# Kernel optimization log

Measured on AMD Instinct MI355X. Metric: run time of the kernel, lower is better.

## Reference

```python
import jax, jax.numpy as jnp
import numpy as np

N = 100000   # num nodes
E = 1200000  # num edges
D = 64       # hidden_channel == middle_channel
ALPHA = 0.5
LN_EPS = 1e-5


def setup_inputs() -> dict:
    key = jax.random.key(0)
    ks = jax.random.split(key, 8)
    z = jax.random.normal(ks[0], (N, D), jnp.float32)
    x = jax.random.normal(ks[1], (N, D), jnp.float32)
    edge_index = jax.random.randint(ks[2], (2, E), 0, N)
    norm_factor = jax.random.uniform(ks[3], (N, 1), jnp.float32)  # >0 a.s.
    s = 0.1
    W = jax.random.normal(ks[4], (D, D), jnp.float32) * s    # nn.Linear(hidden, hidden, bias=False).weight
    U_w = jax.random.normal(ks[5], (D, D), jnp.float32) * s  # nn.Linear(hidden, middle).weight
    U_b = jax.random.normal(ks[6], (D,), jnp.float32) * s    # nn.Linear(hidden, middle).bias
    ln_gamma = jnp.ones((D,), jnp.float32)
    ln_beta = jnp.zeros((D,), jnp.float32)
    return dict(z=z, x=x, edge_index=edge_index, norm_factor=norm_factor,
                W=W, U_w=U_w, U_b=U_b, ln_gamma=ln_gamma, ln_beta=ln_beta)


def reference(z, x, edge_index, norm_factor, W, U_w, U_b, ln_gamma, ln_beta):
    row, col = edge_index[0], edge_index[1]
    # rescale=True: degree = 1/norm_factor with inf -> 0 (safe division)
    safe_nf = jnp.where(norm_factor > 0, norm_factor, 1.0)
    degree = jnp.where(norm_factor > 0, 1.0 / safe_nf, 0.0)  # [N,1]
    # double_linear=True: W(z) + degree * U(x), then graph-norm scale
    WzUx = z @ W.T + degree * (x @ U_w.T + U_b)  # [N,D]
    WzUx = norm_factor * WzUx
    # edge diff (gather), act + LayerNorm (batch=None path)
    e = WzUx[row] - WzUx[col]                    # [E,D]
    e = jax.nn.relu(e)
    mu = jnp.mean(e, axis=-1, keepdims=True)
    var = jnp.var(e, axis=-1, keepdims=True)
    e = (e - mu) * jax.lax.rsqrt(var + LN_EPS) * ln_gamma + ln_beta
    # double scatter_add aggregation
    new_z = jax.ops.segment_sum(e * norm_factor[row], row, num_segments=N)
    new_z = new_z - jax.ops.segment_sum(e * norm_factor[col], col, num_segments=N)
    # -F.linear(new_z, W.t()) == -(new_z @ W)
    new_z = -(new_z @ W)
    # dropout p=0.0 -> identity
    return ALPHA * new_z + (1.0 - ALPHA) * z
```

## Files before the change

kernel.cpp:

```cpp
#include <hip/hip_runtime.h>

#define D 64
#define LN_EPS 1e-5f
#define ALPHA 0.5f

#define GSH 8
#define GBN 256
#define NSUB 8
#define TILE 2048
#define CAPS 1280
#define CAPQ 1792
#define OVF_CAP 131072
#define MAXBUCK 400
#define WZB 2048

__device__ __forceinline__ unsigned xcc_id() {
    unsigned v;
    asm volatile("s_getreg_b32 %0, hwreg(HW_REG_XCC_ID)" : "=s"(v));
    return v & (NSUB - 1);
}

__device__ __forceinline__ unsigned short f2bf(float f) {
    unsigned u = __float_as_uint(f);
    u += 0x7FFF + ((u >> 16) & 1);
    return (unsigned short)(u >> 16);
}
__device__ __forceinline__ float bf2f(unsigned short h) {
    return __uint_as_float(((unsigned)h) << 16);
}

template <int CTRL>
__device__ __forceinline__ float dpp_rotadd(float v) {
    int p = __builtin_amdgcn_update_dpp(0, __float_as_int(v), CTRL, 0xF, 0xF, true);
    return v + __int_as_float(p);
}

__global__ __launch_bounds__(256) void front_kernel(
    const int* __restrict__ row, const int* __restrict__ col,
    int* __restrict__ gcur, int* __restrict__ data,
    int* __restrict__ ovf_cnt, int2* __restrict__ ovf,
    int E, int nbuck, int sb,
    const float* __restrict__ z, const float* __restrict__ x,
    const float* __restrict__ nf, const float* __restrict__ W,
    const float* __restrict__ Uw, const float* __restrict__ Ub,
    unsigned short* __restrict__ wzux, int N)
{
    __shared__ int cnt[MAXBUCK];
    __shared__ int gbase[MAXBUCK];
    const int t = threadIdx.x;

    if ((int)blockIdx.x < sb) {
        const int e0 = blockIdx.x * TILE;
        const int e1 = min(e0 + TILE, E);
        const unsigned sub = xcc_id();

        for (int i = t; i < nbuck; i += 256) cnt[i] = 0;
        __syncthreads();

        for (int e = e0 + t; e < e1; e += 256) {
            atomicAdd(&cnt[row[e] >> GSH], 1);
            atomicAdd(&cnt[col[e] >> GSH], 1);
        }
        __syncthreads();

        for (int b = t; b < nbuck; b += 256) {
            int c = cnt[b];
            gbase[b] = (c > 0) ? atomicAdd(&gcur[b * NSUB + sub], c) : 0;
        }
        __syncthreads();

        for (int e = e0 + t; e < e1; e += 256) {
            int r = row[e], c = col[e];
            {
                int b = r >> GSH;
                int s = atomicSub(&cnt[b], 1) - 1;
                int pos = gbase[b] + s;
                int rec = (c << 9) | ((r & (GBN - 1)) << 1);
                if (pos < CAPS) data[(b * NSUB + (int)sub) * CAPS + pos] = rec;
                else { int o = atomicAdd(ovf_cnt, 1);
                       if (o < OVF_CAP) ovf[o] = make_int2(b, rec); }
            }
            {
                int b = c >> GSH;
                int s = atomicSub(&cnt[b], 1) - 1;
                int pos = gbase[b] + s;
                int rec = (r << 9) | ((c & (GBN - 1)) << 1) | 1;
                if (pos < CAPS) data[(b * NSUB + (int)sub) * CAPS + pos] = rec;
                else { int o = atomicAdd(ovf_cnt, 1);
                       if (o < OVF_CAP) ovf[o] = make_int2(b, rec); }
            }
        }
    } else {
        const int wb   = blockIdx.x - sb;
        const int lane = t & 63;
        const int wid  = t >> 6;
        const int par   = (wb >> 3) & 1;
        const int chunk = (wb & 7) | ((wb >> 4) << 3);
        const int half = lane >> 5;
        const int d    = par * 32 + (lane & 31);

        const float* M = half ? Uw : W;
        float4 wreg[16];
        {
            const float4* wr = (const float4*)(M + (size_t)d * D);
#pragma unroll
            for (int i = 0; i < 16; ++i) wreg[i] = wr[i];
        }
        const float ub = Ub[d];
        const float* base_src = half ? x : z;

        const int start = chunk * 4 + wid;
        const int step  = (WZB >> 1) * 4;

        for (int n = start; n < N; n += step) {
            const int un = __builtin_amdgcn_readfirstlane(n);
            const float4* src = (const float4*)(base_src + (size_t)un * D);
            float a0 = 0.f, a1 = 0.f, a2 = 0.f, a3 = 0.f;
#pragma unroll
            for (int c = 0; c < 16; ++c) {
                float4 v = src[c];
                a0 = fmaf(v.x, wreg[c].x, a0);
                a1 = fmaf(v.y, wreg[c].y, a1);
                a2 = fmaf(v.z, wreg[c].z, a2);
                a3 = fmaf(v.w, wreg[c].w, a3);
            }
            float acc = (a0 + a1) + (a2 + a3);
            float other = __shfl_xor(acc, 32);
            if (half == 0) {
                float nfv = nf[un];
                float deg = (nfv > 0.f) ? (1.f / nfv) : 0.f;
                wzux[(size_t)un * D + d] = f2bf(nfv * (acc + deg * (other + ub)));
            }
        }
    }
}

__global__ __launch_bounds__(256) void bucket_sort_agg_kernel(
    const unsigned short* __restrict__ wzux,
    const int* __restrict__ gcur, const int* __restrict__ data,
    const int* __restrict__ ovf_cnt, const int2* __restrict__ ovf,
    const float* __restrict__ nf,
    const float4* __restrict__ gamma4, const float4* __restrict__ beta4,
    float4* __restrict__ out4, int N)
{
    __shared__ int sorted[CAPQ];
    __shared__ int offs[65];
    __shared__ int curs[64];

    const int blk    = blockIdx.x;
    const int base   = blk << 6;
    const int cntN   = min(64, N - base);
    const int bucket = blk >> 2;
    const int q      = blk & 3;
    const int t      = threadIdx.x;

    if (t < 65) offs[t] = 0;
    __syncthreads();

    const int ocnt = min(*ovf_cnt, OVF_CAP);

    for (int sub = 0; sub < NSUB; ++sub) {
        const int cs = min(gcur[bucket * NSUB + sub], CAPS);
        const int* p = &data[(bucket * NSUB + sub) * CAPS];
        for (int i = t; i < cs; i += 256) {
            int l8 = (p[i] >> 1) & (GBN - 1);
            if ((l8 >> 6) == q) atomicAdd(&offs[(l8 & 63) + 1], 1);
        }
    }
    for (int i = t; i < ocnt; i += 256) {
        int2 v = ovf[i];
        int l8 = (v.y >> 1) & (GBN - 1);
        if (v.x == bucket && (l8 >> 6) == q) atomicAdd(&offs[(l8 & 63) + 1], 1);
    }
    __syncthreads();

    if (t < 64) {
        int v = offs[t + 1];
#pragma unroll
        for (int off = 1; off < 64; off <<= 1) {
            int u = __shfl_up(v, off);
            if (t >= off) v += u;
        }
        offs[t + 1] = v;
    }
    __syncthreads();
    if (t < 64) curs[t] = offs[t];
    __syncthreads();

    for (int sub = 0; sub < NSUB; ++sub) {
        const int cs = min(gcur[bucket * NSUB + sub], CAPS);
        const int* p = &data[(bucket * NSUB + sub) * CAPS];
        for (int i = t; i < cs; i += 256) {
            int rec = p[i];
            int l8 = (rec >> 1) & (GBN - 1);
            if ((l8 >> 6) == q) {
                int pos = atomicAdd(&curs[l8 & 63], 1);
                if (pos < CAPQ) sorted[pos] = rec;
            }
        }
    }
    for (int i = t; i < ocnt; i += 256) {
        int2 v = ovf[i];
        int l8 = (v.y >> 1) & (GBN - 1);
        if (v.x == bucket && (l8 >> 6) == q) {
            int pos = atomicAdd(&curs[l8 & 63], 1);
            if (pos < CAPQ) sorted[pos] = v.y;
        }
    }
    __syncthreads();

    const int lane = t & 63;
    const int wid  = t >> 6;
    const int g = lane >> 4;
    const int l = lane & 15;
    const float4 gm = gamma4[l];
    const float4 bt = beta4[l];
    const ushort4* wz4 = (const ushort4*)wzux;

    for (int local = wid; local < cntN; local += 4) {
        const int s = min(offs[local], CAPQ);
        const int e = min(offs[local + 1], CAPQ);
        const int n = base + local;
        ushort4 sh = wz4[n * 16 + l];
        const float4 self = make_float4(bf2f(sh.x), bf2f(sh.y),
                                        bf2f(sh.z), bf2f(sh.w));
        float4 acc = make_float4(0.f, 0.f, 0.f, 0.f);

#define PROC2(ENT, H)                                                        \
        {                                                                    \
            int ent = (ENT);                                                 \
            float sgn = (ent & 1) ? -1.f : 1.f;                              \
            float4 o = make_float4(bf2f((H).x), bf2f((H).y),                 \
                                   bf2f((H).z), bf2f((H).w));                \
            float r0 = fmaxf(sgn * (self.x - o.x), 0.f);                     \
            float r1 = fmaxf(sgn * (self.y - o.y), 0.f);                     \
            float r2 = fmaxf(sgn * (self.z - o.z), 0.f);                     \
            float r3 = fmaxf(sgn * (self.w - o.w), 0.f);                     \
            float ss = r0 + r1 + r2 + r3;                                    \
            float sq = r0 * r0 + r1 * r1 + r2 * r2 + r3 * r3;                \
            ss = dpp_rotadd<0x128>(ss);  sq = dpp_rotadd<0x128>(sq);         \
            ss = dpp_rotadd<0x124>(ss);  sq = dpp_rotadd<0x124>(sq);         \
            ss = dpp_rotadd<0x122>(ss);  sq = dpp_rotadd<0x122>(sq);         \
            ss = dpp_rotadd<0x121>(ss);  sq = dpp_rotadd<0x121>(sq);         \
            float mu   = ss * (1.f / 64.f);                                  \
            float var  = sq * (1.f / 64.f) - mu * mu;                        \
            float rstd = rsqrtf(var + LN_EPS);                               \
            acc.x += sgn * ((r0 - mu) * rstd * gm.x + bt.x);                 \
            acc.y += sgn * ((r1 - mu) * rstd * gm.y + bt.y);                 \
            acc.z += sgn * ((r2 - mu) * rstd * gm.z + bt.z);                 \
            acc.w += sgn * ((r3 - mu) * rstd * gm.w + bt.w);                 \
        }

        int i = s + g;
        for (; i + 12 < e; i += 16) {
            int e0 = sorted[i];
            int e1 = sorted[i + 4];
            int e2 = sorted[i + 8];
            int e3 = sorted[i + 12];
            ushort4 h0 = wz4[(e0 >> 9) * 16 + l];
            ushort4 h1 = wz4[(e1 >> 9) * 16 + l];
            ushort4 h2 = wz4[(e2 >> 9) * 16 + l];
            ushort4 h3 = wz4[(e3 >> 9) * 16 + l];
            PROC2(e0, h0);
            PROC2(e1, h1);
            PROC2(e2, h2);
            PROC2(e3, h3);
        }
        for (; i < e; i += 4) {
            int e0 = sorted[i];
            ushort4 h0 = wz4[(e0 >> 9) * 16 + l];
            PROC2(e0, h0);
        }
#undef PROC2

#pragma unroll
        for (int m = 16; m < 64; m <<= 1) {
            acc.x += __shfl_xor(acc.x, m);
            acc.y += __shfl_xor(acc.y, m);
            acc.z += __shfl_xor(acc.z, m);
            acc.w += __shfl_xor(acc.w, m);
        }

        if (g == 0) {
            float nfv = nf[n];
            out4[n * 16 + l] = make_float4(acc.x * nfv, acc.y * nfv,
                                           acc.z * nfv, acc.w * nfv);
        }
    }
}

__global__ __launch_bounds__(256) void out_kernel(
    const float* accv, const float* __restrict__ z,
    const float* __restrict__ W, float* out, int N)
{
    const int lane = threadIdx.x & 63;
    const int wid  = threadIdx.x >> 6;

    float wcol[D];
#pragma unroll
    for (int k = 0; k < D; ++k) wcol[k] = W[k * D + lane];

    for (int n = blockIdx.x * 4 + wid; n < N; n += gridDim.x * 4) {
        const int un = __builtin_amdgcn_readfirstlane(n);
        const float4* ar = (const float4*)(accv + (size_t)un * D);
        float a0 = 0.f, a1 = 0.f, a2 = 0.f, a3 = 0.f;
#pragma unroll
        for (int c = 0; c < 16; ++c) {
            float4 a = ar[c];
            a0 = fmaf(a.x, wcol[c * 4 + 0], a0);
            a1 = fmaf(a.y, wcol[c * 4 + 1], a1);
            a2 = fmaf(a.z, wcol[c * 4 + 2], a2);
            a3 = fmaf(a.w, wcol[c * 4 + 3], a3);
        }
        float acc = (a0 + a1) + (a2 + a3);
        out[(size_t)un * D + lane] =
            (1.0f - ALPHA) * z[(size_t)un * D + lane] - ALPHA * acc;
    }
}

extern "C" void kernel_launch(void* const* d_in, const int* in_sizes, int n_in,
                              void* d_out, int out_size, void* d_ws, size_t ws_size,
                              hipStream_t stream) {
    const float* z     = (const float*)d_in[0];
    const float* x     = (const float*)d_in[1];
    const int*   ei    = (const int*)d_in[2];
    const float* nf    = (const float*)d_in[3];
    const float* W     = (const float*)d_in[4];
    const float* Uw    = (const float*)d_in[5];
    const float* Ub    = (const float*)d_in[6];
    const float* gamma = (const float*)d_in[7];
    const float* beta  = (const float*)d_in[8];

    const int N = in_sizes[0] / D;
    const int E = in_sizes[2] / 2;
    const int nbuck = (N + GBN - 1) >> GSH;
    const int sb = (E + TILE - 1) / TILE;

    float* out = (float*)d_out;

    char* ws = (char*)d_ws;
    size_t off = 0;
    auto alloc = [&](size_t bytes) {
        char* p = ws + off;
        off += (bytes + 255) & ~(size_t)255;
        return p;
    };
    unsigned short* wzux = (unsigned short*)alloc((size_t)N * D * 2);
    int*   gcur    = (int*)  alloc((size_t)nbuck * NSUB * sizeof(int));
    int*   ovf_cnt = (int*)  alloc(sizeof(int));
    int*   data    = (int*)  alloc((size_t)nbuck * NSUB * CAPS * sizeof(int));
    int2*  ovf     = (int2*) alloc((size_t)OVF_CAP * sizeof(int2));

    hipMemsetAsync(gcur, 0, (size_t)nbuck * NSUB * sizeof(int), stream);
    hipMemsetAsync(ovf_cnt, 0, sizeof(int), stream);

    front_kernel<<<sb + WZB, 256, 0, stream>>>(
        ei, ei + E, gcur, data, ovf_cnt, ovf, E, nbuck, sb,
        z, x, nf, W, Uw, Ub, wzux, N);

    int ab = (N + 63) / 64;
    bucket_sort_agg_kernel<<<ab, 256, 0, stream>>>(
        wzux, gcur, data, ovf_cnt, ovf, nf,
        (const float4*)gamma, (const float4*)beta,
        (float4*)out, N);

    out_kernel<<<2048, 256, 0, stream>>>(out, z, W, out, N);
}
```

Measured before the change: 337.0 us.

## Replace global-atomic bucket slots with per-block LDS-sorted runs and offset tables

Each edge-tile block now counts its bucket histogram, scans it in LDS, sorts its records locally into shared memory, and writes one contiguous run plus a per-block bucket offset table. This drops the global atomics on per-XCC bucket cursors, the overflow path and the memsets. The aggregation kernel now walks every tile block's offset entry for its bucket, so each thread reads a short serial segment, which may give poorly coalesced reads and load imbalance. The matmul part also pins the weight registers with an empty asm barrier.

```diff
diff --git a/kernel.cpp b/kernel.cpp
--- a/kernel.cpp
+++ b/kernel.cpp
@@ -6,19 +6,13 @@
 
 #define GSH 8
 #define GBN 256
-#define NSUB 8
-#define TILE 2048
-#define CAPS 1280
+#define TILE 1024
+#define RPB  (2*TILE)
 #define CAPQ 1792
-#define OVF_CAP 131072
-#define MAXBUCK 400
+#define MAXB 400
 #define WZB 2048
 
-__device__ __forceinline__ unsigned xcc_id() {
-    unsigned v;
-    asm volatile("s_getreg_b32 %0, hwreg(HW_REG_XCC_ID)" : "=s"(v));
-    return v & (NSUB - 1);
-}
+typedef float vf4 __attribute__((ext_vector_type(4)));
 
 __device__ __forceinline__ unsigned short f2bf(float f) {
     unsigned u = __float_as_uint(f);
@@ -37,59 +31,87 @@
 
 __global__ __launch_bounds__(256) void front_kernel(
     const int* __restrict__ row, const int* __restrict__ col,
-    int* __restrict__ gcur, int* __restrict__ data,
-    int* __restrict__ ovf_cnt, int2* __restrict__ ovf,
+    int* __restrict__ boffs, int* __restrict__ data,
     int E, int nbuck, int sb,
     const float* __restrict__ z, const float* __restrict__ x,
     const float* __restrict__ nf, const float* __restrict__ W,
     const float* __restrict__ Uw, const float* __restrict__ Ub,
     unsigned short* __restrict__ wzux, int N)
 {
-    __shared__ int cnt[MAXBUCK];
-    __shared__ int gbase[MAXBUCK];
+    __shared__ int cnt[MAXB];
+    __shared__ int scn[MAXB + 8];
+    __shared__ int rbuf[RPB];
     const int t = threadIdx.x;
 
     if ((int)blockIdx.x < sb) {
         const int e0 = blockIdx.x * TILE;
         const int e1 = min(e0 + TILE, E);
-        const unsigned sub = xcc_id();
+
+        int rr[4], cc[4];
+#pragma unroll
+        for (int k = 0; k < 4; ++k) {
+            int e = e0 + t + k * 256;
+            bool ok = e < e1;
+            rr[k] = ok ? row[e] : -1;
+            cc[k] = ok ? col[e] : -1;
+        }
 
         for (int i = t; i < nbuck; i += 256) cnt[i] = 0;
         __syncthreads();
 
-        for (int e = e0 + t; e < e1; e += 256) {
-            atomicAdd(&cnt[row[e] >> GSH], 1);
-            atomicAdd(&cnt[col[e] >> GSH], 1);
-        }
-        __syncthreads();
-
-        for (int b = t; b < nbuck; b += 256) {
-            int c = cnt[b];
-            gbase[b] = (c > 0) ? atomicAdd(&gcur[b * NSUB + sub], c) : 0;
-        }
-        __syncthreads();
-
-        for (int e = e0 + t; e < e1; e += 256) {
-            int r = row[e], c = col[e];
-            {
-                int b = r >> GSH;
-                int s = atomicSub(&cnt[b], 1) - 1;
-                int pos = gbase[b] + s;
-                int rec = (c << 9) | ((r & (GBN - 1)) << 1);
-                if (pos < CAPS) data[(b * NSUB + (int)sub) * CAPS + pos] = rec;
-                else { int o = atomicAdd(ovf_cnt, 1);
-                       if (o < OVF_CAP) ovf[o] = make_int2(b, rec); }
-            }
-            {
-                int b = c >> GSH;
-                int s = atomicSub(&cnt[b], 1) - 1;
-                int pos = gbase[b] + s;
-                int rec = (r << 9) | ((c & (GBN - 1)) << 1) | 1;
-                if (pos < CAPS) data[(b * NSUB + (int)sub) * CAPS + pos] = rec;
-                else { int o = atomicAdd(ovf_cnt, 1);
-                       if (o < OVF_CAP) ovf[o] = make_int2(b, rec); }
-            }
-        }
+#pragma unroll
+        for (int k = 0; k < 4; ++k) {
+            if (rr[k] >= 0) {
+                atomicAdd(&cnt[rr[k] >> GSH], 1);
+                atomicAdd(&cnt[cc[k] >> GSH], 1);
+            }
+        }
+        __syncthreads();
+
+        if (t < 64) {
+            int base = t * 7;
+            int loc[7]; int s = 0;
+#pragma unroll
+            for (int j = 0; j < 7; ++j) {
+                int b = base + j;
+                int v = (b < nbuck) ? cnt[b] : 0;
+                loc[j] = s; s += v;
+            }
+            int inc = s;
+#pragma unroll
+            for (int off = 1; off < 64; off <<= 1) {
+                int u = __shfl_up(inc, off);
+                if (t >= off) inc += u;
+            }
+            int excl = inc - s;
+#pragma unroll
+            for (int j = 0; j < 7; ++j) {
+                int b = base + j;
+                if (b <= nbuck) scn[b] = excl + loc[j];
+            }
+        }
+        __syncthreads();
+
+        const int rbase = blockIdx.x * RPB;
+        for (int b = t; b <= nbuck; b += 256)
+            boffs[blockIdx.x * (nbuck + 1) + b] = rbase + scn[b];
+        for (int b = t; b < nbuck; b += 256) cnt[b] = scn[b];
+        __syncthreads();
+
+#pragma unroll
+        for (int k = 0; k < 4; ++k) {
+            int r = rr[k], c = cc[k];
+            if (r >= 0) {
+                rbuf[atomicAdd(&cnt[r >> GSH], 1)] =
+                    (c << 9) | ((r & (GBN - 1)) << 1);
+                rbuf[atomicAdd(&cnt[c >> GSH], 1)] =
+                    (r << 9) | ((c & (GBN - 1)) << 1) | 1;
+            }
+        }
+        __syncthreads();
+
+        const int total = scn[nbuck];
+        for (int i = t; i < total; i += 256) data[rbase + i] = rbuf[i];
     } else {
         const int wb   = blockIdx.x - sb;
         const int lane = t & 63;
@@ -100,9 +122,9 @@
         const int d    = par * 32 + (lane & 31);
 
         const float* M = half ? Uw : W;
-        float4 wreg[16];
+        vf4 wreg[16];
         {
-            const float4* wr = (const float4*)(M + (size_t)d * D);
+            const vf4* wr = (const vf4*)(M + (size_t)d * D);
 #pragma unroll
             for (int i = 0; i < 16; ++i) wreg[i] = wr[i];
         }
@@ -113,12 +135,16 @@
         const int step  = (WZB >> 1) * 4;
 
         for (int n = start; n < N; n += step) {
+#pragma unroll
+            for (int i = 0; i < 16; ++i)
+                asm volatile("" : "+v"(wreg[i]));
+
             const int un = __builtin_amdgcn_readfirstlane(n);
-            const float4* src = (const float4*)(base_src + (size_t)un * D);
+            const vf4* src = (const vf4*)(base_src + (size_t)un * D);
             float a0 = 0.f, a1 = 0.f, a2 = 0.f, a3 = 0.f;
 #pragma unroll
             for (int c = 0; c < 16; ++c) {
-                float4 v = src[c];
+                vf4 v = src[c];
                 a0 = fmaf(v.x, wreg[c].x, a0);
                 a1 = fmaf(v.y, wreg[c].y, a1);
                 a2 = fmaf(v.z, wreg[c].z, a2);
@@ -137,8 +163,8 @@
 
 __global__ __launch_bounds__(256) void bucket_sort_agg_kernel(
     const unsigned short* __restrict__ wzux,
-    const int* __restrict__ gcur, const int* __restrict__ data,
-    const int* __restrict__ ovf_cnt, const int2* __restrict__ ovf,
+    const int* __restrict__ boffs, const int* __restrict__ data,
+    int nblk, int nbuck,
     const float* __restrict__ nf,
     const float4* __restrict__ gamma4, const float4* __restrict__ beta4,
     float4* __restrict__ out4, int N)
@@ -157,20 +183,13 @@
     if (t < 65) offs[t] = 0;
     __syncthreads();
 
-    const int ocnt = min(*ovf_cnt, OVF_CAP);
-
-    for (int sub = 0; sub < NSUB; ++sub) {
-        const int cs = min(gcur[bucket * NSUB + sub], CAPS);
-        const int* p = &data[(bucket * NSUB + sub) * CAPS];
-        for (int i = t; i < cs; i += 256) {
-            int l8 = (p[i] >> 1) & (GBN - 1);
+    for (int b = t; b < nblk; b += 256) {
+        const int* bo = &boffs[b * (nbuck + 1) + bucket];
+        int s0 = bo[0], s1 = bo[1];
+        for (int i = s0; i < s1; ++i) {
+            int l8 = (data[i] >> 1) & (GBN - 1);
             if ((l8 >> 6) == q) atomicAdd(&offs[(l8 & 63) + 1], 1);
         }
-    }
-    for (int i = t; i < ocnt; i += 256) {
-        int2 v = ovf[i];
-        int l8 = (v.y >> 1) & (GBN - 1);
-        if (v.x == bucket && (l8 >> 6) == q) atomicAdd(&offs[(l8 & 63) + 1], 1);
     }
     __syncthreads();
 
@@ -187,24 +206,16 @@
     if (t < 64) curs[t] = offs[t];
     __syncthreads();
 
-    for (int sub = 0; sub < NSUB; ++sub) {
-        const int cs = min(gcur[bucket * NSUB + sub], CAPS);
-        const int* p = &data[(bucket * NSUB + sub) * CAPS];
-        for (int i = t; i < cs; i += 256) {
-            int rec = p[i];
+    for (int b = t; b < nblk; b += 256) {
+        const int* bo = &boffs[b * (nbuck + 1) + bucket];
+        int s0 = bo[0], s1 = bo[1];
+        for (int i = s0; i < s1; ++i) {
+            int rec = data[i];
             int l8 = (rec >> 1) & (GBN - 1);
             if ((l8 >> 6) == q) {
                 int pos = atomicAdd(&curs[l8 & 63], 1);
                 if (pos < CAPQ) sorted[pos] = rec;
             }
-        }
-    }
-    for (int i = t; i < ocnt; i += 256) {
-        int2 v = ovf[i];
-        int l8 = (v.y >> 1) & (GBN - 1);
-        if (v.x == bucket && (l8 >> 6) == q) {
-            int pos = atomicAdd(&curs[l8 & 63], 1);
-            if (pos < CAPQ) sorted[pos] = v.y;
         }
     }
     __syncthreads();
@@ -346,21 +357,16 @@
         return p;
     };
     unsigned short* wzux = (unsigned short*)alloc((size_t)N * D * 2);
-    int*   gcur    = (int*)  alloc((size_t)nbuck * NSUB * sizeof(int));
-    int*   ovf_cnt = (int*)  alloc(sizeof(int));
-    int*   data    = (int*)  alloc((size_t)nbuck * NSUB * CAPS * sizeof(int));
-    int2*  ovf     = (int2*) alloc((size_t)OVF_CAP * sizeof(int2));
-
-    hipMemsetAsync(gcur, 0, (size_t)nbuck * NSUB * sizeof(int), stream);
-    hipMemsetAsync(ovf_cnt, 0, sizeof(int), stream);
+    int* boffs = (int*)alloc((size_t)sb * (nbuck + 1) * sizeof(int));
+    int* data  = (int*)alloc((size_t)sb * RPB * sizeof(int));
 
     front_kernel<<<sb + WZB, 256, 0, stream>>>(
-        ei, ei + E, gcur, data, ovf_cnt, ovf, E, nbuck, sb,
+        ei, ei + E, boffs, data, E, nbuck, sb,
         z, x, nf, W, Uw, Ub, wzux, N);
 
     int ab = (N + 63) / 64;
     bucket_sort_agg_kernel<<<ab, 256, 0, stream>>>(
-        wzux, gcur, data, ovf_cnt, ovf, nf,
+        wzux, boffs, data, sb, nbuck, nf,
         (const float4*)gamma, (const float4*)beta,
         (float4*)out, N);
 
```

Result: slower. 391.7 us (+16.2%).
